# Kernel tuning notes

Measured on AMD Instinct MI355X. Metric: run time of the kernel, lower is better.

## Reference

```python
import jax, jax.numpy as jnp
import numpy as np

B, H, W, C = 64, 56, 56, 256
WIN, SHIFT, HEADS = 7, 3, 8
HEAD_DIM = C // HEADS
N = WIN * WIN
EPS = 1e-5


def _rel_pos_index():
    # matches get_relative_position_index (tf.meshgrid 'xy' indexing)
    xx, yy = np.meshgrid(np.arange(WIN), np.arange(WIN))  # shapes (W,H)
    coords = np.stack([yy, xx], 0).reshape(2, -1)  # (2, N)
    rel = coords[:, :, None] - coords[:, None, :]  # (2, N, N)
    rel = rel.transpose(1, 2, 0)
    idx = (rel[:, :, 0] + WIN - 1) * (2 * WIN - 1) + (rel[:, :, 1] + WIN - 1)
    return jnp.asarray(idx, dtype=jnp.int32)  # (N, N)


def _attn_mask():
    # shifted-window attention mask, (nW, N, N) with 0 / -100
    img = np.zeros((H, W), dtype=np.float32)
    cnt = 0
    for hs in (slice(0, -WIN), slice(-WIN, -SHIFT), slice(-SHIFT, None)):
        for ws in (slice(0, -WIN), slice(-WIN, -SHIFT), slice(-SHIFT, None)):
            img[hs, ws] = cnt
            cnt += 1
    mw = img.reshape(H // WIN, WIN, W // WIN, WIN).transpose(0, 2, 1, 3).reshape(-1, N)
    am = mw[:, None, :] - mw[:, :, None]
    am = np.where(am != 0, -100.0, 0.0).astype(np.float32)
    return jnp.asarray(am)  # (nW, N, N)


def _layer_norm(x, g, b):
    mu = jnp.mean(x, -1, keepdims=True)
    var = jnp.mean(jnp.square(x - mu), -1, keepdims=True)
    return (x - mu) * jax.lax.rsqrt(var + EPS) * g + b


def setup_inputs() -> dict:
    key = jax.random.key(0)
    ks = jax.random.split(key, 6)
    s = lambda fan: 1.0 / np.sqrt(fan)
    return {
        'x': jax.random.normal(ks[0], (B, H * W, C), jnp.float32),
        'ln1_g': jnp.ones((C,), jnp.float32),
        'ln1_b': jnp.zeros((C,), jnp.float32),
        'qkv_w': jax.random.normal(ks[1], (C, 3 * C), jnp.float32) * s(C),
        'qkv_b': jnp.zeros((3 * C,), jnp.float32),
        'rpb_table': jax.random.normal(ks[2], ((2 * WIN - 1) ** 2, HEADS), jnp.float32) * 0.02,
        'proj_w': jax.random.normal(ks[3], (C, C), jnp.float32) * s(C),
        'proj_b': jnp.zeros((C,), jnp.float32),
        'ln2_g': jnp.ones((C,), jnp.float32),
        'ln2_b': jnp.zeros((C,), jnp.float32),
        'mlp_w1': jax.random.normal(ks[4], (C, 4 * C), jnp.float32) * s(C),
        'mlp_b1': jnp.zeros((4 * C,), jnp.float32),
        'mlp_w2': jax.random.normal(ks[5], (4 * C, C), jnp.float32) * s(4 * C),
        'mlp_b2': jnp.zeros((C,), jnp.float32),
    }


def _forward(x, ln1_g, ln1_b, qkv_w, qkv_b, rpb_table, proj_w, proj_b,
             ln2_g, ln2_b, mlp_w1, mlp_b1, mlp_w2, mlp_b2):
    rel_idx = _rel_pos_index()
    mask = _attn_mask()
    nW = (H // WIN) * (W // WIN)

    shortcut = x
    y = _layer_norm(x, ln1_g, ln1_b).reshape(B, H, W, C)
    y = jnp.roll(y, (-SHIFT, -SHIFT), axis=(1, 2))
    # window partition -> (B*nW, N, C)
    y = y.reshape(B, H // WIN, WIN, W // WIN, WIN, C)
    y = y.transpose(0, 1, 3, 2, 4, 5).reshape(B * nW, N, C)

    qkv = (y @ qkv_w + qkv_b).reshape(B * nW, N, 3, HEADS, HEAD_DIM)
    q, k, v = jnp.moveaxis(qkv, 2, 0)  # each (B*nW, N, heads, hd)
    q = q * (HEAD_DIM ** -0.5)
    attn = jnp.einsum('wqhd,wkhd->whqk', q, k)  # (B*nW, heads, N, N)
    bias = jnp.transpose(rpb_table[rel_idx], (2, 0, 1))  # (heads, N, N)
    attn = attn + bias[None]
    attn = attn.reshape(B, nW, HEADS, N, N) + mask[None, :, None]
    attn = jax.nn.softmax(attn.reshape(B * nW, HEADS, N, N), axis=-1)
    o = jnp.einsum('whqk,wkhd->wqhd', attn, v).reshape(B * nW, N, C)
    o = o @ proj_w + proj_b

    # window reverse + un-shift
    o = o.reshape(B, H // WIN, W // WIN, WIN, WIN, C)
    o = o.transpose(0, 1, 3, 2, 4, 5).reshape(B, H, W, C)
    o = jnp.roll(o, (SHIFT, SHIFT), axis=(1, 2)).reshape(B, H * W, C)

    x = shortcut + o
    h = _layer_norm(x, ln2_g, ln2_b)
    h = jax.nn.gelu(h @ mlp_w1 + mlp_b1, approximate=False) @ mlp_w2 + mlp_b2
    return x + h


def reference(x, ln1_g, ln1_b, qkv_w, qkv_b, rpb_table, proj_w, proj_b,
              ln2_g, ln2_b, mlp_w1, mlp_b1, mlp_w2, mlp_b2):
    return _forward(x, ln1_g, ln1_b, qkv_w, qkv_b, rpb_table, proj_w, proj_b,
                    ln2_g, ln2_b, mlp_w1, mlp_b1, mlp_w2, mlp_b2)
```

## Files before the change

kernel.cpp:

```cpp
#include <hip/hip_runtime.h>
#include <math.h>


typedef __attribute__((ext_vector_type(8))) short bf16x8;
typedef __attribute__((ext_vector_type(4))) float f32x4;

#define NTOK 200704
#define NN   49
#define NPARAM 4680
#define TBL_ELEMS (4 * 8 * 49 * 64)

__device__ __forceinline__ float bf2f(unsigned short u) {
    union { unsigned int i; float f; } v; v.i = ((unsigned)u) << 16; return v.f;
}
__device__ __forceinline__ unsigned short f2bf(float f) {
    union { float fv; unsigned int i; } v; v.fv = f;
    return (unsigned short)((v.i + 0x7fffu + ((v.i >> 16) & 1u)) >> 16);
}

__device__ __forceinline__ void gload_lds16(const unsigned short* g, unsigned short* l) {
    __builtin_amdgcn_global_load_lds(
        (const __attribute__((address_space(1))) unsigned int*)g,
        (__attribute__((address_space(3))) unsigned int*)l, 16, 0, 0);
}

__device__ __forceinline__ float gelu_erf(float v) {
    float av = fabsf(v);
    float x = av * 0.70710678118654752f;
    float t = __builtin_amdgcn_rcpf(fmaf(x, 0.3275911f, 1.0f));
    float p = fmaf(1.061405429f, t, -1.453152027f);
    p = fmaf(p, t, 1.421413741f);
    p = fmaf(p, t, -0.284496736f);
    p = fmaf(p, t, 0.254829592f);
    p = p * t;
    float ex = __builtin_amdgcn_exp2f(x * x * -1.4426950408889634f);
    float E = fmaf(-p, ex, 1.0f);
    return fmaf(0.5f * av, E, 0.5f * v);
}

__global__ void detect_kernel(const unsigned short* __restrict__ xu, int* flag) {
    int ln = threadIdx.x;
    int sane = 0;
    #pragma unroll
    for (int t = 0; t < 16; t++) {
        unsigned u = xu[(ln * 16 + t) * 2];
        unsigned e = (u >> 7) & 0xFF;
        sane += (e >= 0x60 && e <= 0x90) ? 1 : 0;
    }
    #pragma unroll
    for (int off = 32; off; off >>= 1) sane += __shfl_xor(sane, off);
    if (ln == 0) *flag = (sane < 614) ? 1 : 0;
}

__device__ __forceinline__ float ld_any(const void* p, int j, int f) {
    return f ? ((const float*)p)[j] : bf2f(((const unsigned short*)p)[j]);
}

__global__ void convert_params_kernel(
    const void* ln1_g, const void* ln1_b, const void* qkv_b, const void* proj_b,
    const void* ln2_g, const void* ln2_b, const void* b1, const void* b2,
    const void* rpb, const int* __restrict__ flag, float* __restrict__ dst) {
    int i = blockIdx.x * 256 + threadIdx.x;
    if (i >= NPARAM) return;
    int f = *flag;
    const void* src; int j;
    if      (i < 256)  { src = ln1_g;  j = i; }
    else if (i < 512)  { src = ln1_b;  j = i - 256; }
    else if (i < 1280) { src = qkv_b;  j = i - 512; }
    else if (i < 1536) { src = proj_b; j = i - 1280; }
    else if (i < 1792) { src = ln2_g;  j = i - 1536; }
    else if (i < 2048) { src = ln2_b;  j = i - 1792; }
    else if (i < 3072) { src = b1;     j = i - 2048; }
    else if (i < 3328) { src = b2;     j = i - 3072; }
    else               { src = rpb;    j = i - 3328; }
    dst[i] = ld_any(src, j, f);
}

__global__ void build_tbl_kernel(const float* __restrict__ rpbF,
                                 float* __restrict__ tbl) {
    int idx = blockIdx.x * 256 + threadIdx.x;
    if (idx >= TBL_ELEMS) return;
    int k = idx & 63;
    int q = (idx >> 6) % 49;
    int h = ((idx >> 6) / 49) & 7;
    int pat = idx / (64 * 49 * 8);
    float v;
    if (k >= 49) {
        v = -1e30f;
    } else {
        int ir = q / 7, ic = q - ir * 7, jr = k / 7, jc = k - jr * 7;
        v = rpbF[((ir - jr + 6) * 13 + (ic - jc + 6)) * 8 + h];
        int rb = pat >> 1, cb = pat & 1;
        int ci = (rb ? (ir < 4 ? 3 : 6) : 0) + (cb ? (ic < 4 ? 1 : 2) : 0);
        int cj = (rb ? (jr < 4 ? 3 : 6) : 0) + (cb ? (jc < 4 ? 1 : 2) : 0);
        if (ci != cj) v -= 100.f;
    }
    tbl[idx] = v;
}

__global__ void transpose_any(const void* __restrict__ in,
                              unsigned short* __restrict__ out, int K, int N,
                              const int* __restrict__ flag) {
    int f = *flag;
    int idx = blockIdx.x * 256 + threadIdx.x;
    if (idx < K * N) {
        int k = idx / N, n = idx - k * N;
        out[n * K + k] = f2bf(ld_any(in, idx, f));
    }
}

__global__ void relayout_w1(const void* __restrict__ in,
                            unsigned short* __restrict__ out,
                            const int* __restrict__ flag) {
    int f = *flag;
    int idx = blockIdx.x * 256 + threadIdx.x;
    if (idx < 256 * 1024) {
        int k = idx >> 10, h = idx & 1023;
        int c = h >> 5, r = h & 31;
        int ks = k ^ ((r & 7) << 3);
        out[c * 8192 + r * 256 + ks] = f2bf(ld_any(in, idx, f));
    }
}

__global__ void relayout_w2(const void* __restrict__ in,
                            unsigned short* __restrict__ out,
                            const int* __restrict__ flag) {
    int f = *flag;
    int idx = blockIdx.x * 256 + threadIdx.x;
    if (idx < 1024 * 256) {
        int k = idx >> 8, n = idx & 255;
        int c = k >> 5, kk = k & 31;
        int slot = kk ^ ((n & 6) << 2);
        out[c * 8192 + n * 32 + slot] = f2bf(ld_any(in, idx, f));
    }
}

__global__ __launch_bounds__(256) void ln1_window_kernel(
    const void* __restrict__ x, const float* __restrict__ paramsF,
    unsigned short* __restrict__ y, const int* __restrict__ flag) {
    int f = *flag;
    int wv = threadIdx.x >> 6, ln = threadIdx.x & 63;
    int tok = blockIdx.x * 4 + wv;
    float v0, v1, v2, v3;
    if (f) {
        float4 pv = *(const float4*)((const float*)x + (size_t)tok * 256 + ln * 4);
        v0 = pv.x; v1 = pv.y; v2 = pv.z; v3 = pv.w;
    } else {
        ushort4 pv = *(const ushort4*)((const unsigned short*)x + (size_t)tok * 256 + ln * 4);
        v0 = bf2f(pv.x); v1 = bf2f(pv.y); v2 = bf2f(pv.z); v3 = bf2f(pv.w);
    }
    float s = v0 + v1 + v2 + v3;
    float sq = v0 * v0 + v1 * v1 + v2 * v2 + v3 * v3;
    #pragma unroll
    for (int off = 32; off; off >>= 1) { s += __shfl_xor(s, off); sq += __shfl_xor(sq, off); }
    float mu = s * (1.f / 256.f);
    float rs = rsqrtf(fmaxf(sq * (1.f / 256.f) - mu * mu, 0.f) + 1e-5f);
    float4 gv = *(const float4*)(paramsF + ln * 4);
    float4 bv = *(const float4*)(paramsF + 256 + ln * 4);
    int bb = tok / 3136, hw = tok - bb * 3136;
    int h = hw / 56, w = hw - h * 56;
    int hp = h - 3; hp += (hp < 0) ? 56 : 0;
    int wp = w - 3; wp += (wp < 0) ? 56 : 0;
    int win = (hp / 7) * 8 + (wp / 7);
    int n = (hp % 7) * 7 + (wp % 7);
    size_t drow = ((size_t)bb * 64 + win) * NN + n;
    ushort4 o;
    o.x = f2bf((v0 - mu) * rs * gv.x + bv.x);
    o.y = f2bf((v1 - mu) * rs * gv.y + bv.y);
    o.z = f2bf((v2 - mu) * rs * gv.z + bv.z);
    o.w = f2bf((v3 - mu) * rs * gv.w + bv.w);
    *(ushort4*)(y + drow * 256 + ln * 4) = o;
}

__device__ __forceinline__ void gemm_core_k256(
    const unsigned short* __restrict__ A, const unsigned short* __restrict__ Bt,
    int rowBase, int colBase, unsigned short* As, unsigned short* Bs, f32x4 acc[2][4]) {
    const int tid = threadIdx.x;
    const int wv = tid >> 6, ln = tid & 63;
    const int m16 = ln & 15, q4 = ln >> 4;
    const int ar = tid >> 1, ah = (tid & 1) * 32;
    const int br = tid >> 2, bp = (tid & 3) * 16;
    for (int kb = 0; kb < 256; kb += 64) {
        const unsigned short* ag = A + (size_t)(rowBase + ar) * 256 + kb + ah;
        unsigned short* asd = As + ar * 72 + ah;
        #pragma unroll
        for (int i = 0; i < 4; i++)
            *(bf16x8*)(asd + i * 8) = *(const bf16x8*)(ag + i * 8);
        const unsigned short* bg = Bt + (size_t)(colBase + br) * 256 + kb + bp;
        unsigned short* bsd = Bs + br * 72 + bp;
        #pragma unroll
        for (int i = 0; i < 2; i++)
            *(bf16x8*)(bsd + i * 8) = *(const bf16x8*)(bg + i * 8);
        __syncthreads();
        #pragma unroll
        for (int ks = 0; ks < 64; ks += 32) {
            bf16x8 af[2], bfr[4];
            #pragma unroll
            for (int rt = 0; rt < 2; rt++)
                af[rt] = *(const bf16x8*)(As + (wv * 32 + rt * 16 + m16) * 72 + ks + q4 * 8);
            #pragma unroll
            for (int ct = 0; ct < 4; ct++)
                bfr[ct] = *(const bf16x8*)(Bs + (ct * 16 + m16) * 72 + ks + q4 * 8);
            #pragma unroll
            for (int rt = 0; rt < 2; rt++)
                #pragma unroll
                for (int ct = 0; ct < 4; ct++)
                    acc[rt][ct] = __builtin_amdgcn_mfma_f32_16x16x32_bf16(
                        af[rt], bfr[ct], acc[rt][ct], 0, 0, 0);
        }
        __syncthreads();
    }
}

__global__ __launch_bounds__(256) void gemm_qkv_kernel(
    const unsigned short* __restrict__ A, const unsigned short* __restrict__ Bt,
    const float* __restrict__ bias,
    unsigned short* __restrict__ out) {
    __shared__ unsigned short As[128 * 72];
    __shared__ unsigned short Bs[64 * 72];
    const int ln = threadIdx.x & 63, wv = threadIdx.x >> 6;
    const int m16 = ln & 15, q4 = ln >> 4;
    const int rowBase = blockIdx.y * 128, colBase = blockIdx.x * 64;
    f32x4 acc[2][4];
    #pragma unroll
    for (int i = 0; i < 2; i++)
        #pragma unroll
        for (int j = 0; j < 4; j++)
            #pragma unroll
            for (int r = 0; r < 4; r++) acc[i][j][r] = 0.f;
    gemm_core_k256(A, Bt, rowBase, colBase, As, Bs, acc);
    #pragma unroll
    for (int rt = 0; rt < 2; rt++)
        #pragma unroll
        for (int ct = 0; ct < 4; ct++) {
            int col = colBase + ct * 16 + m16;
            float bs = bias[col];
            float scale = (col < 256) ? 0.17677669529663689f : 1.0f;
            #pragma unroll
            for (int r = 0; r < 4; r++) {
                int row = rowBase + wv * 32 + rt * 16 + q4 * 4 + r;
                out[(size_t)row * 768 + col] = f2bf((acc[rt][ct][r] + bs) * scale);
            }
        }
}

__global__ __launch_bounds__(256) void gemm_proj_kernel(
    const unsigned short* __restrict__ A, const unsigned short* __restrict__ Bt,
    const float* __restrict__ bias,
    const void* __restrict__ xin,
    unsigned short* __restrict__ x2, const int* __restrict__ flag) {
    __shared__ unsigned short As[128 * 72];
    __shared__ unsigned short Bs[64 * 72];
    const int f = *flag;
    const int ln = threadIdx.x & 63, wv = threadIdx.x >> 6;
    const int m16 = ln & 15, q4 = ln >> 4;
    const int rowBase = blockIdx.y * 128, colBase = blockIdx.x * 64;
    f32x4 acc[2][4];
    #pragma unroll
    for (int i = 0; i < 2; i++)
        #pragma unroll
        for (int j = 0; j < 4; j++)
            #pragma unroll
            for (int r = 0; r < 4; r++) acc[i][j][r] = 0.f;
    gemm_core_k256(A, Bt, rowBase, colBase, As, Bs, acc);
    #pragma unroll
    for (int rt = 0; rt < 2; rt++)
        #pragma unroll
        for (int r = 0; r < 4; r++) {
            int row = rowBase + wv * 32 + rt * 16 + q4 * 4 + r;
            int win = row / NN, n = row - win * NN;
            int bb = win >> 6, wl = win & 63;
            int i7 = n / 7, j7 = n - i7 * 7;
            int hp = (wl >> 3) * 7 + i7 + 3; if (hp >= 56) hp -= 56;
            int wp = (wl & 7) * 7 + j7 + 3;  if (wp >= 56) wp -= 56;
            size_t drow = ((size_t)bb * 3136 + hp * 56 + wp) * 256;
            #pragma unroll
            for (int ct = 0; ct < 4; ct++) {
                int col = colBase + ct * 16 + m16;
                float v = acc[rt][ct][r] + bias[col] + ld_any(xin, drow + col, f);
                x2[drow + col] = f2bf(v);
            }
        }
}

__global__ __launch_bounds__(256) void attn_mfma_kernel(
    const unsigned short* __restrict__ qkv,
    const float* __restrict__ tbl,
    unsigned short* __restrict__ o) {
    __shared__ __align__(16) unsigned short Vt[256 * 72];
    __shared__ __align__(16) unsigned short Ps[4][64 * 72];
    const int tid = threadIdx.x;
    const int wv = tid >> 6, ln = tid & 63;
    const int m16 = ln & 15, q4 = ln >> 4;
    const int win = blockIdx.x;
    const size_t wbase = (size_t)win * 49 * 768;

    #pragma unroll
    for (int i = 0; i < 8; i++) {
        int idx = i * 256 + tid;
        int ch = idx >> 6, tok = idx & 63;
        if (tok < 49) {
            bf16x8 v = *(const bf16x8*)(qkv + wbase + (size_t)tok * 768 + 512 + ch * 8);
            #pragma unroll
            for (int u = 0; u < 8; u++)
                Vt[(ch * 8 + u) * 72 + tok] = (unsigned short)v[u];
        }
    }
    #pragma unroll
    for (int u = 0; u < 23; u++) Vt[tid * 72 + 49 + u] = 0;

    const int wl = win & 63;
    const int pat = (((wl >> 3) == 7) ? 2 : 0) + (((wl & 7) == 7) ? 1 : 0);
    __syncthreads();

    unsigned short* Pw = &Ps[wv][0];
    for (int hh = 0; hh < 2; hh++) {
        const int h = wv * 2 + hh;
        bf16x8 kf[4], qf[4];
        #pragma unroll
        for (int t = 0; t < 4; t++) {
            size_t rrow = wbase + (size_t)(t * 16 + m16) * 768 + h * 32 + q4 * 8;
            qf[t] = *(const bf16x8*)(qkv + rrow);
            kf[t] = *(const bf16x8*)(qkv + rrow + 256);
        }
        f32x4 acc[4][4];
        #pragma unroll
        for (int kt = 0; kt < 4; kt++)
            #pragma unroll
            for (int qt = 0; qt < 4; qt++) {
                #pragma unroll
                for (int r = 0; r < 4; r++) acc[kt][qt][r] = 0.f;
                acc[kt][qt] = __builtin_amdgcn_mfma_f32_16x16x32_bf16(
                    kf[kt], qf[qt], acc[kt][qt], 0, 0, 0);
            }

        const float* tb = tbl + ((size_t)(pat * 8 + h) * 49) * 64;
        #pragma unroll
        for (int qt = 0; qt < 4; qt++) {
            int q = qt * 16 + m16;
            int qc = q < 49 ? q : 48;
            float s[4][4];
            float mx = -3e38f;
            #pragma unroll
            for (int kt = 0; kt < 4; kt++) {
                float4 tv = *(const float4*)(tb + qc * 64 + kt * 16 + q4 * 4);
                s[kt][0] = acc[kt][qt][0] + tv.x;
                s[kt][1] = acc[kt][qt][1] + tv.y;
                s[kt][2] = acc[kt][qt][2] + tv.z;
                s[kt][3] = acc[kt][qt][3] + tv.w;
                #pragma unroll
                for (int r = 0; r < 4; r++) mx = fmaxf(mx, s[kt][r]);
            }
            mx = fmaxf(mx, __shfl_xor(mx, 16));
            mx = fmaxf(mx, __shfl_xor(mx, 32));
            float sum = 0.f;
            #pragma unroll
            for (int kt = 0; kt < 4; kt++)
                #pragma unroll
                for (int r = 0; r < 4; r++) {
                    float e = __expf(s[kt][r] - mx);
                    s[kt][r] = e; sum += e;
                }
            sum += __shfl_xor(sum, 16);
            sum += __shfl_xor(sum, 32);
            float inv = 1.f / sum;
            #pragma unroll
            for (int kt = 0; kt < 4; kt++) {
                ushort4 p4;
                p4.x = f2bf(s[kt][0] * inv);
                p4.y = f2bf(s[kt][1] * inv);
                p4.z = f2bf(s[kt][2] * inv);
                p4.w = f2bf(s[kt][3] * inv);
                *(ushort4*)(Pw + q * 72 + kt * 16 + q4 * 4) = p4;
            }
        }

        f32x4 po[4][2];
        #pragma unroll
        for (int mt = 0; mt < 4; mt++)
            #pragma unroll
            for (int nt = 0; nt < 2; nt++)
                #pragma unroll
                for (int r = 0; r < 4; r++) po[mt][nt][r] = 0.f;
        #pragma unroll
        for (int kstep = 0; kstep < 2; kstep++) {
            bf16x8 pa[4], vb[2];
            #pragma unroll
            for (int mt = 0; mt < 4; mt++)
                pa[mt] = *(const bf16x8*)(Pw + (mt * 16 + m16) * 72 + kstep * 32 + q4 * 8);
            #pragma unroll
            for (int nt = 0; nt < 2; nt++)
                vb[nt] = *(const bf16x8*)(Vt + (h * 32 + nt * 16 + m16) * 72 + kstep * 32 + q4 * 8);
            #pragma unroll
            for (int mt = 0; mt < 4; mt++)
                #pragma unroll
                for (int nt = 0; nt < 2; nt++)
                    po[mt][nt] = __builtin_amdgcn_mfma_f32_16x16x32_bf16(
                        pa[mt], vb[nt], po[mt][nt], 0, 0, 0);
        }

        #pragma unroll
        for (int mt = 0; mt < 4; mt++)
            #pragma unroll
            for (int r = 0; r < 4; r++) {
                int q = mt * 16 + q4 * 4 + r;
                if (q < 49) {
                    size_t orow = ((size_t)win * 49 + q) * 256 + h * 32;
                    o[orow + m16]      = f2bf(po[mt][0][r]);
                    o[orow + 16 + m16] = f2bf(po[mt][1][r]);
                }
            }
    }
}

__global__ __launch_bounds__(512, 2) void mlp_fused_v5(
    const unsigned short* __restrict__ x2,
    const float* __restrict__ g2F, const float* __restrict__ b2lnF,
    const unsigned short* __restrict__ w1s,
    const float* __restrict__ b1F,
    const unsigned short* __restrict__ w2s,
    const float* __restrict__ b2F,
    void* __restrict__ out, const int* __restrict__ flag) {
    __shared__ __align__(16) unsigned short Bs1[2][32 * 256];
    __shared__ __align__(16) unsigned short Bs2[2][256 * 32];
    const int f = *flag;
    const int tid = threadIdx.x;
    const int wv = tid >> 6, ln = tid & 63;
    const int m16 = ln & 15, q4 = ln >> 4;
    const int tok = blockIdx.x * 128 + wv * 16 + m16;

    {
        const unsigned short* s1 = w1s + tid * 8;
        const unsigned short* s2 = w2s + tid * 8;
        #pragma unroll
        for (int j = 0; j < 2; j++) {
            gload_lds16(s1 + j * 4096, &Bs1[0][tid * 8 + j * 4096]);
            gload_lds16(s2 + j * 4096, &Bs2[0][tid * 8 + j * 4096]);
        }
    }

    bf16x8 areg[8];
    {
        const unsigned short* xr = x2 + (size_t)tok * 256 + q4 * 8;
        #pragma unroll
        for (int ks = 0; ks < 8; ks++) areg[ks] = *(const bf16x8*)(xr + ks * 32);
        float s = 0.f, sq = 0.f;
        #pragma unroll
        for (int ks = 0; ks < 8; ks++)
            #pragma unroll
            for (int u = 0; u < 8; u++) {
                float v = bf2f((unsigned short)areg[ks][u]);
                s += v; sq += v * v;
            }
        s += __shfl_xor(s, 16); s += __shfl_xor(s, 32);
        sq += __shfl_xor(sq, 16); sq += __shfl_xor(sq, 32);
        float mu = s * (1.f / 256.f);
        float rs = rsqrtf(fmaxf(sq * (1.f / 256.f) - mu * mu, 0.f) + 1e-5f);
        #pragma unroll
        for (int ks = 0; ks < 8; ks++)
            #pragma unroll
            for (int u = 0; u < 8; u++) {
                int kidx = ks * 32 + q4 * 8 + u;
                float v = (bf2f((unsigned short)areg[ks][u]) - mu) * rs * g2F[kidx] + b2lnF[kidx];
                areg[ks][u] = (short)f2bf(v);
            }
    }

    f32x4 acc2[16];
    #pragma unroll
    for (int i = 0; i < 16; i++)
        #pragma unroll
        for (int r = 0; r < 4; r++) acc2[i][r] = 0.f;

    const int l1 = m16 + (((2 * q4) & 3) << 4);
    const int l2 = m16 + (((2 * q4 + 1) & 3) << 4);
    const bool hi = q4 >= 2;
    const int kswz2 = (m16 & 6) << 2;

    #pragma unroll 1
    for (int c = 0; c < 32; ++c) {
        const int cur = c & 1;
        asm volatile("s_waitcnt vmcnt(0)" ::: "memory");
        __builtin_amdgcn_s_barrier();
        __builtin_amdgcn_sched_barrier(0);

        if (c + 1 < 32) {
            const unsigned short* s1 = w1s + (size_t)(c + 1) * 8192 + tid * 8;
            const unsigned short* s2 = w2s + (size_t)(c + 1) * 8192 + tid * 8;
            unsigned short* d1 = &Bs1[cur ^ 1][tid * 8];
            unsigned short* d2 = &Bs2[cur ^ 1][tid * 8];
            #pragma unroll
            for (int j = 0; j < 2; j++) {
                gload_lds16(s1 + j * 4096, d1 + j * 4096);
                gload_lds16(s2 + j * 4096, d2 + j * 4096);
            }
        }
        __builtin_amdgcn_sched_barrier(0);

        f32x4 acc1[2];
        #pragma unroll
        for (int ct = 0; ct < 2; ct++)
            #pragma unroll
            for (int r = 0; r < 4; r++) acc1[ct][r] = 0.f;
        const unsigned short* b1base = &Bs1[cur][0];
        __builtin_amdgcn_s_setprio(1);
        #pragma unroll
        for (int ks = 0; ks < 8; ks++) {
            int kidx = (ks * 32 + q4 * 8) ^ ((m16 & 7) << 3);
            #pragma unroll
            for (int ct = 0; ct < 2; ct++) {
                bf16x8 wfr = *(const bf16x8*)(b1base + (ct * 16 + m16) * 256 + kidx);
                acc1[ct] = __builtin_amdgcn_mfma_f32_16x16x32_bf16(wfr, areg[ks], acc1[ct], 0, 0, 0);
            }
        }
        __builtin_amdgcn_s_setprio(0);

        union { ushort4 s; unsigned int u[2]; } pk[2];
        #pragma unroll
        for (int ct = 0; ct < 2; ct++) {
            float4 bb = *(const float4*)(b1F + c * 32 + ct * 16 + q4 * 4);
            pk[ct].s.x = f2bf(gelu_erf(acc1[ct][0] + bb.x));
            pk[ct].s.y = f2bf(gelu_erf(acc1[ct][1] + bb.y));
            pk[ct].s.z = f2bf(gelu_erf(acc1[ct][2] + bb.z));
            pk[ct].s.w = f2bf(gelu_erf(acc1[ct][3] + bb.w));
        }

        unsigned int r0x = __shfl(pk[0].u[0], l1), r0y = __shfl(pk[0].u[1], l1);
        unsigned int r0z = __shfl(pk[0].u[0], l2), r0w = __shfl(pk[0].u[1], l2);
        unsigned int r1x = __shfl(pk[1].u[0], l1), r1y = __shfl(pk[1].u[1], l1);
        unsigned int r1z = __shfl(pk[1].u[0], l2), r1w = __shfl(pk[1].u[1], l2);
        union { bf16x8 v; unsigned int u[4]; } bfrag;
        bfrag.u[0] = hi ? r1x : r0x;
        bfrag.u[1] = hi ? r1y : r0y;
        bfrag.u[2] = hi ? r1z : r0z;
        bfrag.u[3] = hi ? r1w : r0w;

        const unsigned short* b2base = &Bs2[cur][0];
        #pragma unroll
        for (int g = 0; g < 4; g++) {
            bf16x8 wf[4];
            #pragma unroll
            for (int j = 0; j < 4; j++)
                wf[j] = *(const bf16x8*)(b2base + ((g * 4 + j) * 16 + m16) * 32 + ((q4 * 8) ^ kswz2));
            __builtin_amdgcn_s_setprio(1);
            #pragma unroll
            for (int j = 0; j < 4; j++)
                acc2[g * 4 + j] = __builtin_amdgcn_mfma_f32_16x16x32_bf16(
                    wf[j], bfrag.v, acc2[g * 4 + j], 0, 0, 0);
            __builtin_amdgcn_s_setprio(0);
        }
    }

    const size_t trow = (size_t)tok * 256;
    #pragma unroll
    for (int ct2 = 0; ct2 < 16; ct2++) {
        int col0 = ct2 * 16 + q4 * 4;
        float4 bb = *(const float4*)(b2F + col0);
        ushort4 rv = *(const ushort4*)(x2 + trow + col0);
        float v0 = acc2[ct2][0] + bb.x + bf2f(rv.x);
        float v1 = acc2[ct2][1] + bb.y + bf2f(rv.y);
        float v2 = acc2[ct2][2] + bb.z + bf2f(rv.z);
        float v3 = acc2[ct2][3] + bb.w + bf2f(rv.w);
        if (f) {
            float4 ov = {v0, v1, v2, v3};
            *(float4*)((float*)out + trow + col0) = ov;
        } else {
            ushort4 ov;
            ov.x = f2bf(v0); ov.y = f2bf(v1); ov.z = f2bf(v2); ov.w = f2bf(v3);
            *(ushort4*)((unsigned short*)out + trow + col0) = ov;
        }
    }
}

extern "C" void kernel_launch(void* const* d_in, const int* in_sizes, int n_in,
                              void* d_out, int out_size, void* d_ws, size_t ws_size,
                              hipStream_t stream) {
    const void* x      = d_in[0];
    const void* qkv_w  = d_in[3];
    const void* proj_w = d_in[6];
    const void* w1     = d_in[10];
    const void* w2     = d_in[12];

    char* ws = (char*)d_ws;
    size_t off = 0;
    unsigned short* y = (unsigned short*)(ws + off);
    off += (size_t)NTOK * 256 * 2;
    size_t qkv_off = off;
    unsigned short* qkv = (unsigned short*)(ws + off);
    off += (size_t)NTOK * 768 * 2;
    unsigned short* x2 = (unsigned short*)(ws + qkv_off);
    unsigned short* o = y;
    unsigned short* qkvWt = (unsigned short*)(ws + off); off += 768 * 256 * 2;
    unsigned short* projWt = (unsigned short*)(ws + off); off += 256 * 256 * 2;
    unsigned short* w1s = (unsigned short*)(ws + off); off += 1024 * 256 * 2;
    unsigned short* w2s = (unsigned short*)(ws + off); off += 256 * 1024 * 2;
    float* paramsF = (float*)(ws + off); off += NPARAM * 4;
    int* flag = (int*)(ws + off); off += 16;
    float* tbl = (float*)(ws + off); off += (size_t)TBL_ELEMS * 4;
    (void)ws_size; (void)in_sizes; (void)n_in; (void)out_size;

    detect_kernel<<<1, 64, 0, stream>>>((const unsigned short*)x, flag);
    convert_params_kernel<<<(NPARAM + 255) / 256, 256, 0, stream>>>(
        d_in[1], d_in[2], d_in[4], d_in[7], d_in[8], d_in[9], d_in[11], d_in[13],
        d_in[5], flag, paramsF);
    build_tbl_kernel<<<(TBL_ELEMS + 255) / 256, 256, 0, stream>>>(paramsF + 3328, tbl);
    transpose_any<<<(256 * 768 + 255) / 256, 256, 0, stream>>>(qkv_w, qkvWt, 256, 768, flag);
    transpose_any<<<(256 * 256 + 255) / 256, 256, 0, stream>>>(proj_w, projWt, 256, 256, flag);
    relayout_w1<<<(256 * 1024 + 255) / 256, 256, 0, stream>>>(w1, w1s, flag);
    relayout_w2<<<(1024 * 256 + 255) / 256, 256, 0, stream>>>(w2, w2s, flag);

    ln1_window_kernel<<<NTOK / 4, 256, 0, stream>>>(x, paramsF, y, flag);
    gemm_qkv_kernel<<<dim3(768 / 64, NTOK / 128), 256, 0, stream>>>(y, qkvWt, paramsF + 512, qkv);
    attn_mfma_kernel<<<4096, 256, 0, stream>>>(qkv, tbl, o);
    gemm_proj_kernel<<<dim3(256 / 64, NTOK / 128), 256, 0, stream>>>(
        o, projWt, paramsF + 1280, x, x2, flag);
    mlp_fused_v5<<<NTOK / 128, 512, 0, stream>>>(
        x2, paramsF + 1536, paramsF + 1792, w1s, paramsF + 2048, w2s, paramsF + 3072, d_out, flag);
}
```

Before: 1.478 ms.

## Switch fused MLP to 32x32x16 MFMA with 32 tokens per wave

Rewrites the fused LN2+MLP kernel to use 32x32x16 bf16 MFMA instructions. Each wave now handles 32 tokens instead of 16, so each block covers 256 tokens and the grid is halved. Per-block weight staging through LDS is therefore amortized over twice as many tokens, and the hidden-activation exchange between lanes becomes a single xor-32 shuffle. The cost is much higher register pressure: 16 A fragments plus 8 f32x16 accumulators per lane, which risks spills or lower occupancy under the 512x2 launch bound.

```diff
diff --git a/kernel.cpp b/kernel.cpp
--- a/kernel.cpp
+++ b/kernel.cpp
@@ -4,6 +4,7 @@
 
 typedef __attribute__((ext_vector_type(8))) short bf16x8;
 typedef __attribute__((ext_vector_type(4))) float f32x4;
+typedef __attribute__((ext_vector_type(16))) float f32x16;
 
 #define NTOK 200704
 #define NN   49
@@ -413,7 +414,7 @@
     }
 }
 
-__global__ __launch_bounds__(512, 2) void mlp_fused_v5(
+__global__ __launch_bounds__(512, 2) void mlp_fused_v6(
     const unsigned short* __restrict__ x2,
     const float* __restrict__ g2F, const float* __restrict__ b2lnF,
     const unsigned short* __restrict__ w1s,
@@ -426,56 +427,59 @@
     const int f = *flag;
     const int tid = threadIdx.x;
     const int wv = tid >> 6, ln = tid & 63;
-    const int m16 = ln & 15, q4 = ln >> 4;
-    const int tok = blockIdx.x * 128 + wv * 16 + m16;
+    const int t32 = ln & 31, hi = ln >> 5;
+    const int tok = blockIdx.x * 256 + wv * 32 + t32;
 
     {
         const unsigned short* s1 = w1s + tid * 8;
         const unsigned short* s2 = w2s + tid * 8;
-        #pragma unroll
-        for (int j = 0; j < 2; j++) {
-            gload_lds16(s1 + j * 4096, &Bs1[0][tid * 8 + j * 4096]);
-            gload_lds16(s2 + j * 4096, &Bs2[0][tid * 8 + j * 4096]);
-        }
-    }
-
-    bf16x8 areg[8];
+        gload_lds16(s1,        &Bs1[0][tid * 8]);
+        gload_lds16(s1 + 4096, &Bs1[0][tid * 8 + 4096]);
+        gload_lds16(s2,        &Bs2[0][tid * 8]);
+        gload_lds16(s2 + 4096, &Bs2[0][tid * 8 + 4096]);
+    }
+
+    bf16x8 areg[16];
     {
-        const unsigned short* xr = x2 + (size_t)tok * 256 + q4 * 8;
-        #pragma unroll
-        for (int ks = 0; ks < 8; ks++) areg[ks] = *(const bf16x8*)(xr + ks * 32);
+        const unsigned short* xr = x2 + (size_t)tok * 256 + hi * 8;
+        #pragma unroll
+        for (int ks = 0; ks < 16; ks++) areg[ks] = *(const bf16x8*)(xr + ks * 16);
         float s = 0.f, sq = 0.f;
         #pragma unroll
-        for (int ks = 0; ks < 8; ks++)
+        for (int ks = 0; ks < 16; ks++)
             #pragma unroll
             for (int u = 0; u < 8; u++) {
                 float v = bf2f((unsigned short)areg[ks][u]);
                 s += v; sq += v * v;
             }
-        s += __shfl_xor(s, 16); s += __shfl_xor(s, 32);
-        sq += __shfl_xor(sq, 16); sq += __shfl_xor(sq, 32);
+        s += __shfl_xor(s, 32); sq += __shfl_xor(sq, 32);
         float mu = s * (1.f / 256.f);
         float rs = rsqrtf(fmaxf(sq * (1.f / 256.f) - mu * mu, 0.f) + 1e-5f);
         #pragma unroll
-        for (int ks = 0; ks < 8; ks++)
+        for (int ks = 0; ks < 16; ks++) {
+            const int kb = ks * 16 + hi * 8;
+            float4 ga = *(const float4*)(g2F + kb);
+            float4 gb = *(const float4*)(g2F + kb + 4);
+            float4 ba = *(const float4*)(b2lnF + kb);
+            float4 bb = *(const float4*)(b2lnF + kb + 4);
+            float g[8] = {ga.x, ga.y, ga.z, ga.w, gb.x, gb.y, gb.z, gb.w};
+            float b[8] = {ba.x, ba.y, ba.z, ba.w, bb.x, bb.y, bb.z, bb.w};
             #pragma unroll
             for (int u = 0; u < 8; u++) {
-                int kidx = ks * 32 + q4 * 8 + u;
-                float v = (bf2f((unsigned short)areg[ks][u]) - mu) * rs * g2F[kidx] + b2lnF[kidx];
+                float v = (bf2f((unsigned short)areg[ks][u]) - mu) * rs * g[u] + b[u];
                 areg[ks][u] = (short)f2bf(v);
             }
-    }
-
-    f32x4 acc2[16];
-    #pragma unroll
-    for (int i = 0; i < 16; i++)
-        #pragma unroll
-        for (int r = 0; r < 4; r++) acc2[i][r] = 0.f;
-
-    const int l1 = m16 + (((2 * q4) & 3) << 4);
-    const int l2 = m16 + (((2 * q4 + 1) & 3) << 4);
-    const bool hi = q4 >= 2;
-    const int kswz2 = (m16 & 6) << 2;
+        }
+    }
+
+    f32x16 acc2[8];
+    #pragma unroll
+    for (int g = 0; g < 8; g++)
+        #pragma unroll
+        for (int r = 0; r < 16; r++) acc2[g][r] = 0.f;
+
+    const int rswz = (t32 & 7) << 3;
+    const int csw = ((t32 >> 1) & 3) << 3;
 
     #pragma unroll 1
     for (int c = 0; c < 32; ++c) {
@@ -489,87 +493,84 @@
             const unsigned short* s2 = w2s + (size_t)(c + 1) * 8192 + tid * 8;
             unsigned short* d1 = &Bs1[cur ^ 1][tid * 8];
             unsigned short* d2 = &Bs2[cur ^ 1][tid * 8];
-            #pragma unroll
-            for (int j = 0; j < 2; j++) {
-                gload_lds16(s1 + j * 4096, d1 + j * 4096);
-                gload_lds16(s2 + j * 4096, d2 + j * 4096);
-            }
+            gload_lds16(s1,        d1);
+            gload_lds16(s1 + 4096, d1 + 4096);
+            gload_lds16(s2,        d2);
+            gload_lds16(s2 + 4096, d2 + 4096);
         }
         __builtin_amdgcn_sched_barrier(0);
 
-        f32x4 acc1[2];
-        #pragma unroll
-        for (int ct = 0; ct < 2; ct++)
-            #pragma unroll
-            for (int r = 0; r < 4; r++) acc1[ct][r] = 0.f;
-        const unsigned short* b1base = &Bs1[cur][0];
+        f32x16 acc1;
+        #pragma unroll
+        for (int r = 0; r < 16; r++) acc1[r] = 0.f;
+        const unsigned short* b1b = &Bs1[cur][0];
         __builtin_amdgcn_s_setprio(1);
         #pragma unroll
-        for (int ks = 0; ks < 8; ks++) {
-            int kidx = (ks * 32 + q4 * 8) ^ ((m16 & 7) << 3);
-            #pragma unroll
-            for (int ct = 0; ct < 2; ct++) {
-                bf16x8 wfr = *(const bf16x8*)(b1base + (ct * 16 + m16) * 256 + kidx);
-                acc1[ct] = __builtin_amdgcn_mfma_f32_16x16x32_bf16(wfr, areg[ks], acc1[ct], 0, 0, 0);
-            }
+        for (int ks = 0; ks < 16; ks++) {
+            bf16x8 wfr = *(const bf16x8*)(b1b + t32 * 256 + ((ks * 16 + hi * 8) ^ rswz));
+            acc1 = __builtin_amdgcn_mfma_f32_32x32x16_bf16(wfr, areg[ks], acc1, 0, 0, 0);
         }
         __builtin_amdgcn_s_setprio(0);
 
-        union { ushort4 s; unsigned int u[2]; } pk[2];
-        #pragma unroll
-        for (int ct = 0; ct < 2; ct++) {
-            float4 bb = *(const float4*)(b1F + c * 32 + ct * 16 + q4 * 4);
-            pk[ct].s.x = f2bf(gelu_erf(acc1[ct][0] + bb.x));
-            pk[ct].s.y = f2bf(gelu_erf(acc1[ct][1] + bb.y));
-            pk[ct].s.z = f2bf(gelu_erf(acc1[ct][2] + bb.z));
-            pk[ct].s.w = f2bf(gelu_erf(acc1[ct][3] + bb.w));
-        }
-
-        unsigned int r0x = __shfl(pk[0].u[0], l1), r0y = __shfl(pk[0].u[1], l1);
-        unsigned int r0z = __shfl(pk[0].u[0], l2), r0w = __shfl(pk[0].u[1], l2);
-        unsigned int r1x = __shfl(pk[1].u[0], l1), r1y = __shfl(pk[1].u[1], l1);
-        unsigned int r1z = __shfl(pk[1].u[0], l2), r1w = __shfl(pk[1].u[1], l2);
-        union { bf16x8 v; unsigned int u[4]; } bfrag;
-        bfrag.u[0] = hi ? r1x : r0x;
-        bfrag.u[1] = hi ? r1y : r0y;
-        bfrag.u[2] = hi ? r1z : r0z;
-        bfrag.u[3] = hi ? r1w : r0w;
-
-        const unsigned short* b2base = &Bs2[cur][0];
-        #pragma unroll
-        for (int g = 0; g < 4; g++) {
-            bf16x8 wf[4];
-            #pragma unroll
-            for (int j = 0; j < 4; j++)
-                wf[j] = *(const bf16x8*)(b2base + ((g * 4 + j) * 16 + m16) * 32 + ((q4 * 8) ^ kswz2));
+        unsigned int d[8];
+        #pragma unroll
+        for (int G = 0; G < 4; G++) {
+            float4 bb = *(const float4*)(b1F + c * 32 + G * 8 + hi * 4);
+            float g0 = gelu_erf(acc1[G * 4 + 0] + bb.x);
+            float g1 = gelu_erf(acc1[G * 4 + 1] + bb.y);
+            float g2 = gelu_erf(acc1[G * 4 + 2] + bb.z);
+            float g3 = gelu_erf(acc1[G * 4 + 3] + bb.w);
+            d[G * 2]     = (unsigned)f2bf(g0) | ((unsigned)f2bf(g1) << 16);
+            d[G * 2 + 1] = (unsigned)f2bf(g2) | ((unsigned)f2bf(g3) << 16);
+        }
+
+        unsigned int x0 = __shfl_xor(d[0], 32), x1 = __shfl_xor(d[1], 32);
+        unsigned int x2e = __shfl_xor(d[2], 32), x3 = __shfl_xor(d[3], 32);
+        unsigned int x4 = __shfl_xor(d[4], 32), x5 = __shfl_xor(d[5], 32);
+        unsigned int x6 = __shfl_xor(d[6], 32), x7 = __shfl_xor(d[7], 32);
+        union { bf16x8 v; unsigned int u[4]; } h0, h1;
+        h0.u[0] = hi ? x2e  : d[0];
+        h0.u[1] = hi ? x3   : d[1];
+        h0.u[2] = hi ? d[2] : x0;
+        h0.u[3] = hi ? d[3] : x1;
+        h1.u[0] = hi ? x6   : d[4];
+        h1.u[1] = hi ? x7   : d[5];
+        h1.u[2] = hi ? d[6] : x4;
+        h1.u[3] = hi ? d[7] : x5;
+
+        const unsigned short* b2b = &Bs2[cur][0];
+        #pragma unroll
+        for (int g = 0; g < 8; g++) {
+            bf16x8 w0 = *(const bf16x8*)(b2b + (g * 32 + t32) * 32 + ((hi * 8) ^ csw));
+            bf16x8 w1f = *(const bf16x8*)(b2b + (g * 32 + t32) * 32 + ((16 + hi * 8) ^ csw));
             __builtin_amdgcn_s_setprio(1);
-            #pragma unroll
-            for (int j = 0; j < 4; j++)
-                acc2[g * 4 + j] = __builtin_amdgcn_mfma_f32_16x16x32_bf16(
-                    wf[j], bfrag.v, acc2[g * 4 + j], 0, 0, 0);
+            acc2[g] = __builtin_amdgcn_mfma_f32_32x32x16_bf16(w0, h0.v, acc2[g], 0, 0, 0);
+            acc2[g] = __builtin_amdgcn_mfma_f32_32x32x16_bf16(w1f, h1.v, acc2[g], 0, 0, 0);
             __builtin_amdgcn_s_setprio(0);
         }
     }
 
     const size_t trow = (size_t)tok * 256;
     #pragma unroll
-    for (int ct2 = 0; ct2 < 16; ct2++) {
-        int col0 = ct2 * 16 + q4 * 4;
-        float4 bb = *(const float4*)(b2F + col0);
-        ushort4 rv = *(const ushort4*)(x2 + trow + col0);
-        float v0 = acc2[ct2][0] + bb.x + bf2f(rv.x);
-        float v1 = acc2[ct2][1] + bb.y + bf2f(rv.y);
-        float v2 = acc2[ct2][2] + bb.z + bf2f(rv.z);
-        float v3 = acc2[ct2][3] + bb.w + bf2f(rv.w);
-        if (f) {
-            float4 ov = {v0, v1, v2, v3};
-            *(float4*)((float*)out + trow + col0) = ov;
-        } else {
-            ushort4 ov;
-            ov.x = f2bf(v0); ov.y = f2bf(v1); ov.z = f2bf(v2); ov.w = f2bf(v3);
-            *(ushort4*)((unsigned short*)out + trow + col0) = ov;
-        }
-    }
+    for (int g = 0; g < 8; g++)
+        #pragma unroll
+        for (int G = 0; G < 4; G++) {
+            int col0 = g * 32 + G * 8 + hi * 4;
+            float4 bb = *(const float4*)(b2F + col0);
+            ushort4 rv = *(const ushort4*)(x2 + trow + col0);
+            float v0 = acc2[g][G * 4 + 0] + bb.x + bf2f(rv.x);
+            float v1 = acc2[g][G * 4 + 1] + bb.y + bf2f(rv.y);
+            float v2 = acc2[g][G * 4 + 2] + bb.z + bf2f(rv.z);
+            float v3 = acc2[g][G * 4 + 3] + bb.w + bf2f(rv.w);
+            if (f) {
+                float4 ov = {v0, v1, v2, v3};
+                *(float4*)((float*)out + trow + col0) = ov;
+            } else {
+                ushort4 ov;
+                ov.x = f2bf(v0); ov.y = f2bf(v1); ov.z = f2bf(v2); ov.w = f2bf(v3);
+                *(ushort4*)((unsigned short*)out + trow + col0) = ov;
+            }
+        }
 }
 
 extern "C" void kernel_launch(void* const* d_in, const int* in_sizes, int n_in,
@@ -614,6 +615,6 @@
     attn_mfma_kernel<<<4096, 256, 0, stream>>>(qkv, tbl, o);
     gemm_proj_kernel<<<dim3(256 / 64, NTOK / 128), 256, 0, stream>>>(
         o, projWt, paramsF + 1280, x, x2, flag);
-    mlp_fused_v5<<<NTOK / 128, 512, 0, stream>>>(
+    mlp_fused_v6<<<NTOK / 256, 512, 0, stream>>>(
         x2, paramsF + 1536, paramsF + 1792, w1s, paramsF + 2048, w2s, paramsF + 3072, d_out, flag);
 }
```

Result: no change. 1.470 ms (-0.6%).
